# Kernel tuning notes

Hardware: AMD Instinct MI355X
Metric: run time of the kernel (lower is better)

The kernel has to match this reference:

```python
import jax, jax.numpy as jnp
import numpy as np

D = 20          # embedding dim (hardcoded in original module)
N_REL = 200     # relation vocab size (table has N_REL+1 rows)
N_TIME = 365    # time embedding table size
L = 3           # propagation layers
E = 2_000_000   # edges per layer
N = 1_000_000   # node-slot pool per layer
B = 64          # batch size
N_ENT = 1_000_003


def setup_inputs() -> dict:
    key = jax.random.key(0)
    ks = jax.random.split(key, 16)
    src_idx = jax.random.randint(ks[0], (L, E), 0, N, dtype=jnp.int32)
    dst_idx = jax.random.randint(ks[1], (L, E), 0, N, dtype=jnp.int32)
    rel_idx = jax.random.randint(ks[2], (L, E), 0, N_REL + 1, dtype=jnp.int32)
    qrel_idx = jax.random.randint(ks[3], (L, E), 0, N_REL + 1, dtype=jnp.int32)
    # signed relative time (edge_time - query_time); abs() must stay < N_TIME
    rel_time = jax.random.randint(ks[4], (L, E), -(N_TIME - 1), N_TIME, dtype=jnp.int32)
    node_batch = jax.random.randint(ks[5], (N,), 0, B, dtype=jnp.int32)
    node_ent = jnp.arange(N, dtype=jnp.int32)  # unique entity per final node slot
    s = 0.1
    rela_embed = jax.random.normal(ks[6], (N_REL + 1, D), jnp.float32) * s
    time_embed = jax.random.normal(ks[7], (N_TIME, D), jnp.float32) * s
    w_att1 = jax.random.normal(ks[8], (30, 3 * D), jnp.float32) * s
    w_att2 = jax.random.normal(ks[9], (1, 30), jnp.float32) * s
    w_past = jax.random.normal(ks[10], (D, D), jnp.float32) * s
    w_now = jax.random.normal(ks[11], (D, D), jnp.float32) * s
    w_future = jax.random.normal(ks[12], (D, D), jnp.float32) * s
    w_cls = jax.random.normal(ks[13], (D,), jnp.float32) * s
    b_cls = jnp.zeros((), jnp.float32)
    return dict(src_idx=src_idx, dst_idx=dst_idx, rel_idx=rel_idx,
                qrel_idx=qrel_idx, rel_time=rel_time, node_batch=node_batch,
                node_ent=node_ent, rela_embed=rela_embed, time_embed=time_embed,
                w_att1=w_att1, w_att2=w_att2, w_past=w_past, w_now=w_now,
                w_future=w_future, w_cls=w_cls, b_cls=b_cls,
                batch_size=B, n_ent=N_ENT)


def reference(src_idx, dst_idx, rel_idx, qrel_idx, rel_time, node_batch,
              node_ent, rela_embed, time_embed, w_att1, w_att2, w_past,
              w_now, w_future, w_cls, b_cls, batch_size, n_ent):
    n_layers = src_idx.shape[0]
    n_nodes = node_batch.shape[0]
    d = rela_embed.shape[1]
    hidden = jnp.zeros((n_nodes, d), dtype=rela_embed.dtype)
    for l in range(n_layers):
        rt = rel_time[l]                         # [E] signed relative time
        h_src = hidden[src_idx[l]]               # [E, D] gather
        r_emb = rela_embed[rel_idx[l]]           # [E, D]
        t_emb = time_embed[jnp.abs(rt)]          # [E, D]
        embed_rel = h_src + r_emb + t_emb
        # conditional time-branch MLP (mask-partitioned linear, same math as
        # the original's boolean-masked assignments)
        fut = embed_rel @ w_future.T
        now = embed_rel @ w_now.T
        pst = embed_rel @ w_past.T
        transformed = jnp.where((rt > 0)[:, None], fut,
                       jnp.where((rt == 0)[:, None], now, pst))
        # attention over concat(hidden_src, rel_emb, query_rel_emb)  [E, 3D]
        att_in = jnp.concatenate([h_src, r_emb, rela_embed[qrel_idx[l]]], axis=1)
        score = jax.nn.sigmoid(jax.nn.relu(att_in @ w_att1.T) @ w_att2.T)  # [E,1]
        msg = score * transformed                # [E, D]
        hidden = jax.ops.segment_sum(msg, dst_idx[l], num_segments=n_nodes)
        hidden = jax.nn.leaky_relu(hidden)       # default slope 0.01, as torch
    result = hidden @ w_cls + b_cls              # [N]
    score_all = jnp.zeros((batch_size, n_ent), dtype=result.dtype)
    score_all = score_all.at[node_batch, node_ent].set(result)
    return score_all
```

## Files before the change

kernel.cpp:

```cpp
#include <hip/hip_runtime.h>
#include <hip/hip_bf16.h>
#include <cstdint>

#define DD 20
#define HID 30
#define NB_SCAN 1024
#define HROW 32

typedef unsigned int  u32;
typedef unsigned short u16;

__device__ __forceinline__ void load20(const float* __restrict__ p, float* r){
  const float4* q = (const float4*)p;
#pragma unroll
  for (int i=0;i<5;i++){ float4 v=q[i]; r[4*i+0]=v.x; r[4*i+1]=v.y; r[4*i+2]=v.z; r[4*i+3]=v.w; }
}

__device__ __forceinline__ u32 pkbf(float a, float b){
  u32 ua=__float_as_uint(a); ua=(ua+0x7FFFu+((ua>>16)&1u))>>16;
  u32 ub=__float_as_uint(b); ub=(ub+0x7FFFu+((ub>>16)&1u))>>16;
  return ua | (ub<<16);
}

__global__ void k_prep(const float* __restrict__ rela, const float* __restrict__ w1,
                       const float* __restrict__ wp, const float* __restrict__ wn,
                       const float* __restrict__ wf,
                       float* __restrict__ W3, float* __restrict__ AR, float* __restrict__ AQ,
                       int nrel){
  int t = blockIdx.x*blockDim.x + threadIdx.x;
  if (t < 3*DD*DD){
    int s = t/(DD*DD), idx = t%(DD*DD);
    W3[t] = (s==0)?wp[idx]:((s==1)?wn[idx]:wf[idx]);
  }
  if (t < nrel*HID){
    int r=t/HID, j=t-r*HID;
    float sr=0.f, sq=0.f;
#pragma unroll
    for (int k=0;k<DD;k++){
      float e = rela[r*DD+k];
      sr += e*w1[j*3*DD + DD + k];
      sq += e*w1[j*3*DD + 2*DD + k];
    }
    AR[r*32+j]=sr; AQ[r*32+j]=sq;
  }
}

__global__ void k_rwtw(const float* __restrict__ rela, const float* __restrict__ timee,
                       const float* __restrict__ W3,
                       float* __restrict__ RW, float* __restrict__ TW,
                       int nrel, int ntime){
  int t = blockIdx.x*blockDim.x+threadIdx.x;
  int totR = 3*nrel*DD, totT = 3*ntime*DD;
  if (t < totR){
    int sel = t/(nrel*DD); int rem = t - sel*nrel*DD; int r = rem/DD; int i = rem - r*DD;
    const float* w = W3 + sel*DD*DD + i*DD;
    const float* e = rela + (size_t)r*DD;
    float s=0.f;
#pragma unroll
    for (int k=0;k<DD;k++) s += e[k]*w[k];
    RW[t]=s;
  }
  if (t < totT){
    int sel = t/(ntime*DD); int rem = t - sel*ntime*DD; int tt = rem/DD; int i = rem - tt*DD;
    const float* w = W3 + sel*DD*DD + i*DD;
    const float* e = timee + (size_t)tt*DD;
    float s=0.f;
#pragma unroll
    for (int k=0;k<DD;k++) s += e[k]*w[k];
    TW[t]=s;
  }
}

__global__ void k_rt(const float* __restrict__ rela, const float* __restrict__ timee,
                     const float* __restrict__ W3, float* __restrict__ RT,
                     int nrel, int ntime){
  int row = blockIdx.x*blockDim.x+threadIdx.x;
  int tot = 3*nrel*ntime;
  if (row>=tot) return;
  int per = nrel*ntime;
  int sel = row/per; int rem = row - sel*per; int r = rem/ntime; int t = rem - r*ntime;
  float e[DD], tv[DD];
  load20(rela + (size_t)r*DD, e);
  load20(timee + (size_t)t*DD, tv);
#pragma unroll
  for (int k=0;k<DD;k++) e[k]+=tv[k];
  const float* W = W3 + sel*DD*DD;
  float o[DD];
#pragma unroll
  for (int i=0;i<DD;i++){
    const float4* wr = (const float4*)(W + i*DD);
    float s=0.f;
#pragma unroll
    for (int c=0;c<5;c++){ float4 w=wr[c]; s += e[4*c]*w.x + e[4*c+1]*w.y + e[4*c+2]*w.z + e[4*c+3]*w.w; }
    o[i]=s;
  }
  float4* op=(float4*)(RT + (size_t)row*DD);
#pragma unroll
  for (int c=0;c<5;c++){ float4 v; v.x=o[4*c]; v.y=o[4*c+1]; v.z=o[4*c+2]; v.w=o[4*c+3]; op[c]=v; }
}

__global__ void __launch_bounds__(256) k_pre(const int* __restrict__ dst0, int* __restrict__ cnt0,
        int* __restrict__ rank0, int E,
        float4* __restrict__ dout4, size_t nd4,
        uint4* __restrict__ b0, uint4* __restrict__ b1, size_t nbB4,
        float4* __restrict__ bF, size_t nf4){
  int g=blockIdx.x, tid=threadIdx.x;
  int half=gridDim.x>>1;
  if (g & 1){
    int stride=half*256;
    for (int e=(g>>1)*256+tid; e<E; e+=stride)
      rank0[e]=atomicAdd(&cnt0[dst0[e]],1);
  } else {
    float4 z=make_float4(0.f,0.f,0.f,0.f);
    uint4 zu=make_uint4(0u,0u,0u,0u);
    size_t i=(size_t)(g>>1)*256+tid, st=(size_t)half*256;
    for (size_t k=i;k<nd4;k+=st) dout4[k]=z;
    for (size_t k=i;k<nbB4;k+=st){ b0[k]=zu; b1[k]=zu; }
    for (size_t k=i;k<nf4;k+=st) bF[k]=z;
  }
}

__global__ void k_scan_part(const int* __restrict__ cnt, int* __restrict__ part, int M, int C){
  __shared__ int sm[256];
  int b=blockIdx.x, t=threadIdx.x;
  int lo=b*C, hi=lo+C; if (hi>M) hi=M; if (lo>M) lo=M;
  int s=0;
  for (int i=lo+t; i<hi; i+=256) s+=cnt[i];
  sm[t]=s; __syncthreads();
  for (int o=128;o>0;o>>=1){ if (t<o) sm[t]+=sm[t+o]; __syncthreads(); }
  if (t==0) part[b]=sm[0];
}

__global__ void k_scan_top(int* __restrict__ part, int* __restrict__ listc){
  __shared__ int sm[NB_SCAN];
  int t=threadIdx.x;
  if (t==0) *listc=0;
  int v=part[t]; sm[t]=v; __syncthreads();
  for (int o=1;o<NB_SCAN;o<<=1){
    int u=(t>=o)?sm[t-o]:0; __syncthreads();
    sm[t]+=u; __syncthreads();
  }
  part[t]=sm[t]-v;
}

__global__ void k_scan_write(const int* __restrict__ cnt, const int* __restrict__ part,
                             int* __restrict__ rowptr, int M, int C){
  __shared__ int sm[256];
  int b=blockIdx.x, t=threadIdx.x;
  int lo=b*C, hi=lo+C; if (hi>M) hi=M; if (lo>M) lo=M;
  int run=part[b];
  for (int base=lo; base<hi; base+=256){
    int i=base+t;
    int v=(i<hi)?cnt[i]:0;
    sm[t]=v; __syncthreads();
    for (int o=1;o<256;o<<=1){
      int u=(t>=o)?sm[t-o]:0; __syncthreads();
      sm[t]+=u; __syncthreads();
    }
    if (i<hi) rowptr[i]=run+sm[t]-v;
    int tot=sm[255];
    __syncthreads();
    run+=tot;
  }
  if (hi==M && t==0) rowptr[M]=run;
}

__global__ void __launch_bounds__(256) k_scat(const int* __restrict__ src,const int* __restrict__ dst,
  const int* __restrict__ rel,const int* __restrict__ qrel,const int* __restrict__ rtm,
  const int* __restrict__ rank,const int* __restrict__ rowptr,int4* __restrict__ recs,int E,
  int xb,
  float* __restrict__ dout,const int* __restrict__ nb,const int* __restrict__ ne,
  const int* __restrict__ nentp,const float* __restrict__ bcls,int N){
  int g=blockIdx.x, tid=threadIdx.x;
  if (g<xb){
    float b=bcls[0]; long long stride=nentp[0];
    for (int n=g*256+tid;n<N;n+=xb*256) dout[(long long)nb[n]*stride+ne[n]]=b;
    return;
  }
  int e=(g-xb)*256+tid;
  if (e>=E) return;
  int d=dst[e];
  int pos=rowptr[d]+rank[e];
  recs[pos]=make_int4(src[e], rel[e]|(qrel[e]<<16), rtm[e], d);
}

template<bool HASH,bool HIST,bool FINAL>
__global__ void __launch_bounds__(256) k_fused(
    const int4* __restrict__ recs,
    const u16* __restrict__ hin, u16* __restrict__ hout, float* __restrict__ bufF,
    const float* __restrict__ RW, const float* __restrict__ TW,
    const float* __restrict__ AR, const float* __restrict__ AQ,
    const float* __restrict__ w1, const float* __restrict__ w2, const float* __restrict__ W3,
    int E, int nrel, int ntime,
    const int* __restrict__ ndst, int* __restrict__ ncnt, int* __restrict__ nrank, int nE,
    const float* __restrict__ wcls, const float* __restrict__ bcls,
    const int* __restrict__ nbv, const int* __restrict__ nev, const int* __restrict__ nentp,
    float* __restrict__ outp, int* __restrict__ list, int* __restrict__ listc)
{
  int lb;
  if (HIST){
    int g=blockIdx.x;
    int r3=g%3, b3=g/3;
    if (r3==2){
      int H=gridDim.x/3;
      int stride=H*256;
      for (int e=b3*256+threadIdx.x; e<nE; e+=stride)
        nrank[e]=atomicAdd(&ncnt[ndst[e]],1);
      return;
    }
    lb=b3*2+r3;
  } else lb=blockIdx.x;
  int bstart=lb*256;
  if (bstart>=E) return;

  __shared__ float sW1h[HID*DD];
  __shared__ float sW2[32];
  __shared__ float sW3[3*DD*DD];
  __shared__ u32   smsg[256*10];
  __shared__ int   sdst[256];
  __shared__ int   s_prevdst, s_nextdst;
  if (HASH){
    for (int t=threadIdx.x; t<HID*DD; t+=blockDim.x){ int j=t/DD,k=t-j*DD; sW1h[t]=w1[j*3*DD+k]; }
    for (int t=threadIdx.x; t<3*DD*DD; t+=blockDim.x) sW3[t]=W3[t];
  }
  if (threadIdx.x<HID) sW2[threadIdx.x]=w2[threadIdx.x];

  int tid = threadIdx.x;
  int bsize = E - bstart; if (bsize>256) bsize=256;
  int j = bstart + tid;
  bool active = (tid < bsize);

  if (tid==0){
    s_prevdst = (bstart>0) ? recs[-1 + (ptrdiff_t)bstart].w : -1;
    s_nextdst = (bstart+bsize < E) ? recs[bstart+bsize].w : -1;
  }
  __syncthreads();

  int dstv = -1;
  float m[DD];
  if (active){
    int4 rc = recs[j];
    int s = rc.x;
    int r = rc.y & 0xFFFF;
    int q = ((unsigned)rc.y) >> 16;
    int t = rc.z;
    dstv  = rc.w;
    int sel = (t>0)?2:((t==0)?1:0);
    int ta = (t<0)?-t:t;

    float h[DD];
    if (HASH){
      const uint4* hp=(const uint4*)(hin+(size_t)s*HROW);
      uint4 A=hp[0], B=hp[1]; uint2 Cc=*((const uint2*)(hp+2));
      h[0]=__uint_as_float(A.x<<16);  h[1]=__uint_as_float(A.x&0xFFFF0000u);
      h[2]=__uint_as_float(A.y<<16);  h[3]=__uint_as_float(A.y&0xFFFF0000u);
      h[4]=__uint_as_float(A.z<<16);  h[5]=__uint_as_float(A.z&0xFFFF0000u);
      h[6]=__uint_as_float(A.w<<16);  h[7]=__uint_as_float(A.w&0xFFFF0000u);
      h[8]=__uint_as_float(B.x<<16);  h[9]=__uint_as_float(B.x&0xFFFF0000u);
      h[10]=__uint_as_float(B.y<<16); h[11]=__uint_as_float(B.y&0xFFFF0000u);
      h[12]=__uint_as_float(B.z<<16); h[13]=__uint_as_float(B.z&0xFFFF0000u);
      h[14]=__uint_as_float(B.w<<16); h[15]=__uint_as_float(B.w&0xFFFF0000u);
      h[16]=__uint_as_float(Cc.x<<16);h[17]=__uint_as_float(Cc.x&0xFFFF0000u);
      h[18]=__uint_as_float(Cc.y<<16);h[19]=__uint_as_float(Cc.y&0xFFFF0000u);
    }

    float z=0.f;
    {
      const float4* ap=(const float4*)(AR+(size_t)r*32);
      const float4* qp=(const float4*)(AQ+(size_t)q*32);
#pragma unroll
      for (int c=0;c<7;c++){
        float4 x=ap[c], y=qp[c];
        float s4[4]={x.x+y.x, x.y+y.y, x.z+y.z, x.w+y.w};
#pragma unroll
        for (int u=0;u<4;u++){
          int jj=4*c+u;
          if (HASH){
            const float4* wr=(const float4*)&sW1h[jj*DD];
            float sum=s4[u];
#pragma unroll
            for (int c2=0;c2<5;c2++){ float4 w=wr[c2]; sum += h[4*c2]*w.x+h[4*c2+1]*w.y+h[4*c2+2]*w.z+h[4*c2+3]*w.w; }
            s4[u]=sum;
          }
          z += fmaxf(s4[u],0.f)*sW2[jj];
        }
      }
      float2 x2=*(const float2*)(AR+(size_t)r*32+28);
      float2 y2=*(const float2*)(AQ+(size_t)q*32+28);
      float s0=x2.x+y2.x, s1=x2.y+y2.y;
      if (HASH){
        const float4* wr0=(const float4*)&sW1h[28*DD];
        const float4* wr1=(const float4*)&sW1h[29*DD];
#pragma unroll
        for (int c2=0;c2<5;c2++){
          float4 wA=wr0[c2], wB=wr1[c2];
          s0 += h[4*c2]*wA.x+h[4*c2+1]*wA.y+h[4*c2+2]*wA.z+h[4*c2+3]*wA.w;
          s1 += h[4*c2]*wB.x+h[4*c2+1]*wB.y+h[4*c2+2]*wB.z+h[4*c2+3]*wB.w;
        }
      }
      z += fmaxf(s0,0.f)*sW2[28] + fmaxf(s1,0.f)*sW2[29];
    }
    float score = 1.f/(1.f+__expf(-z));

    const float4* rwp=(const float4*)(RW + ((size_t)(sel*nrel+r))*DD);
    const float4* twp=(const float4*)(TW + ((size_t)(sel*ntime+ta))*DD);
#pragma unroll
    for (int c=0;c<5;c++){
      float4 a4=rwp[c], b4=twp[c];
      float mv[4]={a4.x+b4.x, a4.y+b4.y, a4.z+b4.z, a4.w+b4.w};
      if (HASH){
#pragma unroll
        for (int u=0;u<4;u++){
          const float4* wr=(const float4*)&sW3[sel*DD*DD+(4*c+u)*DD];
          float sum=mv[u];
#pragma unroll
          for (int c2=0;c2<5;c2++){ float4 w=wr[c2]; sum += h[4*c2]*w.x+h[4*c2+1]*w.y+h[4*c2+2]*w.z+h[4*c2+3]*w.w; }
          mv[u]=sum;
        }
      }
#pragma unroll
      for (int u=0;u<4;u++) m[4*c+u]=score*mv[u];
    }
#pragma unroll
    for (int i2=0;i2<10;i2++) smsg[tid*10+i2]=pkbf(m[2*i2],m[2*i2+1]);
  }
  sdst[tid] = active ? dstv : -2;
  __syncthreads();

  if (!active) return;
  bool isHead = (tid==0) ? (s_prevdst != dstv) : (sdst[tid-1] != dstv);
  if (!(isHead || tid==0)) return;
  int k=tid+1;
  for (; k<bsize && sdst[k]==dstv; ++k){
    const u32* row=&smsg[k*10];
#pragma unroll
    for (int i2=0;i2<10;i2++){
      u32 w=row[i2];
      m[2*i2]  +=__uint_as_float(w<<16);
      m[2*i2+1]+=__uint_as_float(w&0xFFFF0000u);
    }
  }
  bool crossStart = (tid==0 && !isHead);
  bool crossEnd   = (k==bsize) && (s_nextdst==dstv);
  if (crossStart || crossEnd){
    float* o = bufF + (size_t)dstv*DD;
#pragma unroll
    for (int i=0;i<DD;i++) atomicAdd(o+i, m[i]);
    if (isHead){
      int p = atomicAdd(listc,1);
      list[p] = dstv;
    }
  } else {
    if (!FINAL){
      u32 o10[10];
#pragma unroll
      for (int i2=0;i2<10;i2++){
        float x0=m[2*i2], x1=m[2*i2+1];
        x0=fmaxf(x0,0.01f*x0); x1=fmaxf(x1,0.01f*x1);
        o10[i2]=pkbf(x0,x1);
      }
      uint4* hp=(uint4*)(hout+(size_t)dstv*HROW);
      hp[0]=make_uint4(o10[0],o10[1],o10[2],o10[3]);
      hp[1]=make_uint4(o10[4],o10[5],o10[6],o10[7]);
      *((uint2*)(hp+2))=make_uint2(o10[8],o10[9]);
    } else {
      float rsum=bcls[0];
#pragma unroll
      for (int i=0;i<DD;i++){ float x=fmaxf(m[i],0.01f*m[i]); rsum += x*wcls[i]; }
      long long stride = nentp[0];
      outp[(long long)nbv[dstv]*stride + nev[dstv]] = rsum;
    }
  }
}

template<bool FINAL>
__global__ void __launch_bounds__(256) k_fixup(float* __restrict__ bufF, u16* __restrict__ hout,
   const float* __restrict__ wcls,const float* __restrict__ bcls,
   const int* __restrict__ nb,const int* __restrict__ ne,const int* __restrict__ nentp,
   float* __restrict__ out,const int* __restrict__ list,const int* __restrict__ listc){
  int c=*listc;
  for (int i=blockIdx.x*blockDim.x+threadIdx.x; i<c; i+=gridDim.x*blockDim.x){
    int n=list[i];
    float* p=bufF+(size_t)n*DD;
    float v[DD];
#pragma unroll
    for (int jj=0;jj<DD;jj++){ v[jj]=p[jj]; p[jj]=0.f; }
    if (FINAL){
      float rsum=bcls[0];
#pragma unroll
      for (int jj=0;jj<DD;jj++){ float x=fmaxf(v[jj],0.01f*v[jj]); rsum+=x*wcls[jj]; }
      long long stride=nentp[0];
      out[(long long)nb[n]*stride+ne[n]]=rsum;
    } else {
      u32 o10[10];
#pragma unroll
      for (int i2=0;i2<10;i2++){
        float x0=v[2*i2], x1=v[2*i2+1];
        x0=fmaxf(x0,0.01f*x0); x1=fmaxf(x1,0.01f*x1);
        o10[i2]=pkbf(x0,x1);
      }
      uint4* hp=(uint4*)(hout+(size_t)n*HROW);
      hp[0]=make_uint4(o10[0],o10[1],o10[2],o10[3]);
      hp[1]=make_uint4(o10[4],o10[5],o10[6],o10[7]);
      *((uint2*)(hp+2))=make_uint2(o10[8],o10[9]);
    }
  }
}

template<bool HASH>
__global__ void __launch_bounds__(256) k_edge(
    const int* __restrict__ src, const int* __restrict__ dst,
    const int* __restrict__ rel, const int* __restrict__ qrel,
    const int* __restrict__ rtm,
    const float* __restrict__ hin, float* __restrict__ hout,
    const float* __restrict__ RT, const float* __restrict__ AR, const float* __restrict__ AQ,
    const float* __restrict__ w1, const float* __restrict__ w2, const float* __restrict__ W3,
    int E, int nrel, int ntime)
{
  __shared__ float sW1h[HID*DD];
  __shared__ float sW2[32];
  __shared__ float sW3[3*DD*DD];
  for (int t=threadIdx.x; t<HID*DD; t+=blockDim.x){ int j=t/DD,k=t-j*DD; sW1h[t]=w1[j*3*DD+k]; }
  if (threadIdx.x<HID) sW2[threadIdx.x]=w2[threadIdx.x];
  for (int t=threadIdx.x; t<3*DD*DD; t+=blockDim.x) sW3[t]=W3[t];
  __syncthreads();
  int e = blockIdx.x*blockDim.x+threadIdx.x;
  if (e>=E) return;
  int s=src[e], d=dst[e], r=rel[e], q=qrel[e], t=rtm[e];
  int sel = (t>0)?2:((t==0)?1:0);
  int ta = (t<0)?-t:t;
  float h[DD];
  if (HASH){
    load20(hin+(size_t)s*DD, h);
#pragma unroll
    for (int i=0;i<DD;i++) h[i]=fmaxf(h[i],0.01f*h[i]);
  }
  float a[HID];
  {
    const float4* ap=(const float4*)(AR+(size_t)r*32);
    const float4* qp=(const float4*)(AQ+(size_t)q*32);
#pragma unroll
    for (int c=0;c<7;c++){
      float4 x=ap[c], y=qp[c];
      a[4*c+0]=x.x+y.x; a[4*c+1]=x.y+y.y; a[4*c+2]=x.z+y.z; a[4*c+3]=x.w+y.w;
    }
    float2 x=*(const float2*)(AR+(size_t)r*32+28);
    float2 y=*(const float2*)(AQ+(size_t)q*32+28);
    a[28]=x.x+y.x; a[29]=x.y+y.y;
  }
  if (HASH){
#pragma unroll
    for (int j=0;j<HID;j++){
      const float4* wr=(const float4*)&sW1h[j*DD];
      float sum=a[j];
#pragma unroll
      for (int c=0;c<5;c++){ float4 w=wr[c]; sum += h[4*c]*w.x+h[4*c+1]*w.y+h[4*c+2]*w.z+h[4*c+3]*w.w; }
      a[j]=sum;
    }
  }
// ... 36 lines not shown
}

__global__ void k_scatter(const float* __restrict__ res, const int* __restrict__ nb,
                          const int* __restrict__ ne, const int* __restrict__ nentp,
                          float* __restrict__ out, int N){
  int i=blockIdx.x*blockDim.x+threadIdx.x;
  if (i>=N) return;
  long long stride = nentp[0];
  out[(long long)nb[i]*stride + ne[i]] = res[i];
}

extern "C" void kernel_launch(void* const* d_in, const int* in_sizes, int n_in,
                              void* d_out, int out_size, void* d_ws, size_t ws_size,
                              hipStream_t stream){
  const int*   src =(const int*)d_in[0];
  const int*   dst =(const int*)d_in[1];
  const int*   rel =(const int*)d_in[2];
  const int*   qrel=(const int*)d_in[3];
  const int*   rtm =(const int*)d_in[4];
  const int*   nb  =(const int*)d_in[5];
  const int*   ne  =(const int*)d_in[6];
  const float* rela=(const float*)d_in[7];
  const float* timee=(const float*)d_in[8];
  const float* w1  =(const float*)d_in[9];
  const float* w2  =(const float*)d_in[10];
  const float* wp  =(const float*)d_in[11];
  const float* wn  =(const float*)d_in[12];
  const float* wf  =(const float*)d_in[13];
  const float* wcls=(const float*)d_in[14];
  const float* bcls=(const float*)d_in[15];
  const int*   nentp=(const int*)d_in[17];

  const int Lc=3;
  int LE=in_sizes[0]; int E=LE/Lc;
  int N=in_sizes[5];
  int nrel=in_sizes[7]/DD;
  int ntime=in_sizes[8]/DD;

  auto al=[](size_t x){ return (x+(size_t)255)&~(size_t)255; };
  size_t szBufB=al((size_t)N*HROW*2);
  size_t szBufF=al((size_t)N*DD*4);
  size_t szBuf =al((size_t)N*DD*4);
  size_t szRW  =al((size_t)3*nrel*DD*4);
  size_t szTW  =al((size_t)3*ntime*DD*4);
  size_t szRTf =al((size_t)3*nrel*ntime*DD*4);
  size_t szA   =al((size_t)nrel*32*4);
  size_t szW3  =al((size_t)3*DD*DD*4);
  size_t szRow =al((size_t)Lc*((size_t)N+1)*4);
  size_t szRank=al((size_t)LE*4);
  size_t szCnt =al((size_t)Lc*N*4);
  size_t szRecs=al((size_t)LE*16);
  size_t szPart=al((size_t)NB_SCAN*4);
  size_t szList=al((size_t)(131072+16)*4);
  size_t need = 2*szBufB+szBufF+szRW+szTW+2*szA+szW3+szRow+szRank+szCnt+szRecs+szPart+szList;

  dim3 blk(256);
  int prepTot = (3*DD*DD > nrel*HID) ? 3*DD*DD : nrel*HID;
  int rtTot=3*nrel*ntime;
  int rwtwTot = 3*ntime*DD;

  if (ws_size >= need){
    char* base=(char*)d_ws;
    size_t off=0;
    u16*   b0 =(u16*)(base+off);   off+=szBufB;
    u16*   b1 =(u16*)(base+off);   off+=szBufB;
    float* bufF=(float*)(base+off); off+=szBufF;
    float* RW  =(float*)(base+off); off+=szRW;
    float* TW  =(float*)(base+off); off+=szTW;
    float* AR  =(float*)(base+off); off+=szA;
    float* AQ  =(float*)(base+off); off+=szA;
    float* W3  =(float*)(base+off); off+=szW3;
    int*   rowptr=(int*)(base+off); off+=szRow;
    int*   rank=(int*)(base+off);  off+=szRank;
    int*   cnt =(int*)(base+off);  off+=szCnt;
    int4*  recs=(int4*)(base+off); off+=szRecs;
    int*   part=(int*)(base+off);  off+=szPart;
    int*   listc=(int*)(base+off);
    int*   list =listc+16;          off+=szList;

    float* dout=(float*)d_out;

    (void)hipMemsetAsync(cnt,0,(size_t)Lc*N*4,stream);
    k_prep<<<dim3((prepTot+255)/256),blk,0,stream>>>(rela,w1,wp,wn,wf,W3,AR,AQ,nrel);
    k_rwtw<<<dim3((rwtwTot+255)/256),blk,0,stream>>>(rela,timee,W3,RW,TW,nrel,ntime);

    size_t nd4=(size_t)out_size>>2;
    size_t nbB4=(size_t)N*HROW*2/16;
    size_t nf4=(size_t)N*DD/4;
    k_pre<<<dim3(8192),blk,0,stream>>>(dst,cnt,rank,E,(float4*)dout,nd4,
                                       (uint4*)b0,(uint4*)b1,nbB4,(float4*)bufF,nf4);

    int C=(N+NB_SCAN-1)/NB_SCAN;
    int LB=(E+255)/256;
    int H=(LB+1)/2;

    for (int l=0;l<Lc;++l){
      int* cnt_l = cnt + (size_t)l*N;
      int* row_l = rowptr + (size_t)l*(N+1);
      k_scan_part<<<dim3(NB_SCAN),blk,0,stream>>>(cnt_l,part,N,C);
      k_scan_top<<<dim3(1),dim3(NB_SCAN),0,stream>>>(part,listc);
      k_scan_write<<<dim3(NB_SCAN),blk,0,stream>>>(cnt_l,part,row_l,N,C);
      size_t eo=(size_t)l*E;
      int xb = (l==0)?1024:0;
      k_scat<<<dim3(xb+LB),blk,0,stream>>>(src+eo,dst+eo,rel+eo,qrel+eo,rtm+eo,
          rank+eo,row_l,recs+eo,E,xb,dout,nb,ne,nentp,bcls,N);
      if (l==0){
        k_fused<false,true,false><<<dim3(3*H),blk,0,stream>>>(recs,nullptr,b0,bufF,
            RW,TW,AR,AQ,w1,w2,W3,E,nrel,ntime,
            dst+(size_t)E,cnt+(size_t)N,rank+(size_t)E,E,
            nullptr,nullptr,nullptr,nullptr,nullptr,nullptr,list,listc);
        k_fixup<false><<<dim3(128),blk,0,stream>>>(bufF,b0,wcls,bcls,nb,ne,nentp,dout,list,listc);
      } else if (l==1){
        k_fused<true,true,false><<<dim3(3*H),blk,0,stream>>>(recs+(size_t)E,b0,b1,bufF,
            RW,TW,AR,AQ,w1,w2,W3,E,nrel,ntime,
            dst+(size_t)2*E,cnt+(size_t)2*N,rank+(size_t)2*E,E,
            nullptr,nullptr,nullptr,nullptr,nullptr,nullptr,list,listc);
        k_fixup<false><<<dim3(128),blk,0,stream>>>(bufF,b1,wcls,bcls,nb,ne,nentp,dout,list,listc);
      } else {
        k_fused<true,false,true><<<dim3(LB),blk,0,stream>>>(recs+(size_t)2*E,b1,nullptr,bufF,
            RW,TW,AR,AQ,w1,w2,W3,E,nrel,ntime,
            nullptr,nullptr,nullptr,0,
            wcls,bcls,nb,ne,nentp,dout,list,listc);
        k_fixup<true><<<dim3(128),blk,0,stream>>>(bufF,nullptr,wcls,bcls,nb,ne,nentp,dout,list,listc);
      }
    }
  } else {
    char* base=(char*)d_out; float* res=(float*)d_ws;
    size_t off=0;
    float* buf0=(float*)(base+off); off+=szBuf;
    float* buf1=(float*)(base+off); off+=szBuf;
    float* RT  =(float*)(base+off); off+=szRTf;
    float* AR  =(float*)(base+off); off+=szA;
    float* AQ  =(float*)(base+off); off+=szA;
    float* W3  =(float*)(base+off); off+=szW3;
    k_prep<<<dim3((prepTot+255)/256),blk,0,stream>>>(rela,w1,wp,wn,wf,W3,AR,AQ,nrel);
    k_rt<<<dim3((rtTot+255)/256),blk,0,stream>>>(rela,timee,W3,RT,nrel,ntime);
    dim3 egrid((E+255)/256);
    dim3 ngrid((N+255)/256);
    (void)hipMemsetAsync(buf0,0,(size_t)N*DD*4,stream);
    k_edge<false><<<egrid,blk,0,stream>>>(src,dst,rel,qrel,rtm,nullptr,buf0,RT,AR,AQ,w1,w2,W3,E,nrel,ntime);
    (void)hipMemsetAsync(buf1,0,(size_t)N*DD*4,stream);
    k_edge<true><<<egrid,blk,0,stream>>>(src+(size_t)E,dst+(size_t)E,rel+(size_t)E,qrel+(size_t)E,rtm+(size_t)E,
                                         buf0,buf1,RT,AR,AQ,w1,w2,W3,E,nrel,ntime);
    (void)hipMemsetAsync(buf0,0,(size_t)N*DD*4,stream);
    k_edge<true><<<egrid,blk,0,stream>>>(src+(size_t)2*E,dst+(size_t)2*E,rel+(size_t)2*E,qrel+(size_t)2*E,rtm+(size_t)2*E,
                                         buf1,buf0,RT,AR,AQ,w1,w2,W3,E,nrel,ntime);
    k_result<<<ngrid,blk,0,stream>>>(buf0,wcls,bcls,res,N);
    (void)hipMemsetAsync(d_out,0,(size_t)out_size*sizeof(float),stream);
    k_scatter<<<ngrid,blk,0,stream>>>(res,nb,ne,nentp,(float*)d_out,N);
  }
}
```

Measured before the change: 1.057 ms.

## Make fused edge kernel persistent with software-prefetched next tile

```diff
diff --git a/kernel.cpp b/kernel.cpp
--- a/kernel.cpp
+++ b/kernel.cpp
@@ -6,6 +6,7 @@
 #define HID 30
 #define NB_SCAN 1024
 #define HROW 32
+#define CBLK 1024
 
 typedef unsigned int  u32;
 typedef unsigned short u16;
@@ -197,179 +198,209 @@
     const int* __restrict__ nbv, const int* __restrict__ nev, const int* __restrict__ nentp,
     float* __restrict__ outp, int* __restrict__ list, int* __restrict__ listc)
 {
-  int lb;
+  int g=blockIdx.x;
+  int C;
   if (HIST){
-    int g=blockIdx.x;
-    int r3=g%3, b3=g/3;
-    if (r3==2){
-      int H=gridDim.x/3;
-      int stride=H*256;
-      for (int e=b3*256+threadIdx.x; e<nE; e+=stride)
+    if (g & 1){
+      int Hst=gridDim.x>>1;
+      int stride=Hst*256;
+      for (int e=(g>>1)*256+threadIdx.x; e<nE; e+=stride)
         nrank[e]=atomicAdd(&ncnt[ndst[e]],1);
       return;
     }
-    lb=b3*2+r3;
-  } else lb=blockIdx.x;
-  int bstart=lb*256;
-  if (bstart>=E) return;
+    g>>=1; C=gridDim.x>>1;
+  } else C=gridDim.x;
+
+  int nt=(E+255)/256;
+  if (g>=nt) return;
 
   __shared__ float sW1h[HID*DD];
   __shared__ float sW2[32];
   __shared__ float sW3[3*DD*DD];
   __shared__ u32   smsg[256*10];
   __shared__ int   sdst[256];
-  __shared__ int   s_prevdst, s_nextdst;
+  __shared__ int   sPN[2];
+  int tid=threadIdx.x;
   if (HASH){
-    for (int t=threadIdx.x; t<HID*DD; t+=blockDim.x){ int j=t/DD,k=t-j*DD; sW1h[t]=w1[j*3*DD+k]; }
-    for (int t=threadIdx.x; t<3*DD*DD; t+=blockDim.x) sW3[t]=W3[t];
-  }
-  if (threadIdx.x<HID) sW2[threadIdx.x]=w2[threadIdx.x];
-
-  int tid = threadIdx.x;
-  int bsize = E - bstart; if (bsize>256) bsize=256;
-  int j = bstart + tid;
-  bool active = (tid < bsize);
-
-  if (tid==0){
-    s_prevdst = (bstart>0) ? recs[-1 + (ptrdiff_t)bstart].w : -1;
-    s_nextdst = (bstart+bsize < E) ? recs[bstart+bsize].w : -1;
-  }
+    for (int t=tid; t<HID*DD; t+=256){ int j=t/DD,k=t-j*DD; sW1h[t]=w1[j*3*DD+k]; }
+    for (int t=tid; t<3*DD*DD; t+=256) sW3[t]=W3[t];
+  }
+  if (tid<HID) sW2[tid]=w2[tid];
   __syncthreads();
 
-  int dstv = -1;
-  float m[DD];
-  if (active){
-    int4 rc = recs[j];
-    int s = rc.x;
-    int r = rc.y & 0xFFFF;
-    int q = ((unsigned)rc.y) >> 16;
-    int t = rc.z;
-    dstv  = rc.w;
-    int sel = (t>0)?2:((t==0)?1:0);
-    int ta = (t<0)?-t:t;
-
+  int tile=g;
+  int bstart=tile*256;
+  bool act=(bstart+tid<E);
+  int4 rcC = act ? recs[bstart+tid] : make_int4(0,0,0,-2);
+  uint4 hA, hB; uint2 hC2;
+  if (HASH){
+    const uint4* hp=(const uint4*)(hin+(size_t)(act?rcC.x:0)*HROW);
+    hA=hp[0]; hB=hp[1]; hC2=*((const uint2*)(hp+2));
+  }
+
+  while (true){
+    int bsize=E-bstart; if (bsize>256) bsize=256;
+    int tileN=tile+C;
+    int bstartN=tileN*256;
+    bool actN=(tileN<nt)&&(bstartN+tid<E);
+    int4 rcN = actN ? recs[bstartN+tid] : make_int4(0,0,0,-2);
+    if (tid==0){
+      sPN[0]=(bstart>0)?recs[bstart-1].w:-1;
+      sPN[1]=(bstart+bsize<E)?recs[bstart+bsize].w:-1;
+    }
+
+    int dstv=-2;
+    float score=0.f; int sel=0, r=0, q=0, ta=0;
     float h[DD];
+    if (act){
+      dstv=rcC.w;
+      r = rcC.y & 0xFFFF;
+      q = ((unsigned)rcC.y) >> 16;
+      int t = rcC.z;
+      sel = (t>0)?2:((t==0)?1:0);
+      ta = (t<0)?-t:t;
+      if (HASH){
+        h[0]=__uint_as_float(hA.x<<16);  h[1]=__uint_as_float(hA.x&0xFFFF0000u);
+        h[2]=__uint_as_float(hA.y<<16);  h[3]=__uint_as_float(hA.y&0xFFFF0000u);
+        h[4]=__uint_as_float(hA.z<<16);  h[5]=__uint_as_float(hA.z&0xFFFF0000u);
+        h[6]=__uint_as_float(hA.w<<16);  h[7]=__uint_as_float(hA.w&0xFFFF0000u);
+        h[8]=__uint_as_float(hB.x<<16);  h[9]=__uint_as_float(hB.x&0xFFFF0000u);
+        h[10]=__uint_as_float(hB.y<<16); h[11]=__uint_as_float(hB.y&0xFFFF0000u);
+        h[12]=__uint_as_float(hB.z<<16); h[13]=__uint_as_float(hB.z&0xFFFF0000u);
+        h[14]=__uint_as_float(hB.w<<16); h[15]=__uint_as_float(hB.w&0xFFFF0000u);
+        h[16]=__uint_as_float(hC2.x<<16);h[17]=__uint_as_float(hC2.x&0xFFFF0000u);
+        h[18]=__uint_as_float(hC2.y<<16);h[19]=__uint_as_float(hC2.y&0xFFFF0000u);
+      }
+      float z=0.f;
+      {
+        const float4* ap=(const float4*)(AR+(size_t)r*32);
+        const float4* qp=(const float4*)(AQ+(size_t)q*32);
+#pragma unroll
+        for (int c=0;c<7;c++){
+          float4 x=ap[c], y=qp[c];
+          float s4[4]={x.x+y.x, x.y+y.y, x.z+y.z, x.w+y.w};
+#pragma unroll
+          for (int u=0;u<4;u++){
+            int jj=4*c+u;
+            if (HASH){
+              const float4* wr=(const float4*)&sW1h[jj*DD];
+              float sum=s4[u];
+#pragma unroll
+              for (int c2=0;c2<5;c2++){ float4 w=wr[c2]; sum += h[4*c2]*w.x+h[4*c2+1]*w.y+h[4*c2+2]*w.z+h[4*c2+3]*w.w; }
+              s4[u]=sum;
+            }
+            z += fmaxf(s4[u],0.f)*sW2[jj];
+          }
+        }
+        float2 x2=*(const float2*)(AR+(size_t)r*32+28);
+        float2 y2=*(const float2*)(AQ+(size_t)q*32+28);
+        float s0=x2.x+y2.x, s1=x2.y+y2.y;
+        if (HASH){
+          const float4* wr0=(const float4*)&sW1h[28*DD];
+          const float4* wr1=(const float4*)&sW1h[29*DD];
+#pragma unroll
+          for (int c2=0;c2<5;c2++){
+            float4 wA=wr0[c2], wB=wr1[c2];
+            s0 += h[4*c2]*wA.x+h[4*c2+1]*wA.y+h[4*c2+2]*wA.z+h[4*c2+3]*wA.w;
+            s1 += h[4*c2]*wB.x+h[4*c2+1]*wB.y+h[4*c2+2]*wB.z+h[4*c2+3]*wB.w;
+          }
+        }
+        z += fmaxf(s0,0.f)*sW2[28] + fmaxf(s1,0.f)*sW2[29];
+      }
+      score = 1.f/(1.f+__expf(-z));
+    }
+
+    uint4 hAn, hBn; uint2 hCn;
     if (HASH){
-      const uint4* hp=(const uint4*)(hin+(size_t)s*HROW);
-      uint4 A=hp[0], B=hp[1]; uint2 Cc=*((const uint2*)(hp+2));
-      h[0]=__uint_as_float(A.x<<16);  h[1]=__uint_as_float(A.x&0xFFFF0000u);
-      h[2]=__uint_as_float(A.y<<16);  h[3]=__uint_as_float(A.y&0xFFFF0000u);
-      h[4]=__uint_as_float(A.z<<16);  h[5]=__uint_as_float(A.z&0xFFFF0000u);
-      h[6]=__uint_as_float(A.w<<16);  h[7]=__uint_as_float(A.w&0xFFFF0000u);
-      h[8]=__uint_as_float(B.x<<16);  h[9]=__uint_as_float(B.x&0xFFFF0000u);
-      h[10]=__uint_as_float(B.y<<16); h[11]=__uint_as_float(B.y&0xFFFF0000u);
-      h[12]=__uint_as_float(B.z<<16); h[13]=__uint_as_float(B.z&0xFFFF0000u);
-      h[14]=__uint_as_float(B.w<<16); h[15]=__uint_as_float(B.w&0xFFFF0000u);
-      h[16]=__uint_as_float(Cc.x<<16);h[17]=__uint_as_float(Cc.x&0xFFFF0000u);
-      h[18]=__uint_as_float(Cc.y<<16);h[19]=__uint_as_float(Cc.y&0xFFFF0000u);
-    }
-
-    float z=0.f;
-    {
-      const float4* ap=(const float4*)(AR+(size_t)r*32);
-      const float4* qp=(const float4*)(AQ+(size_t)q*32);
-#pragma unroll
-      for (int c=0;c<7;c++){
-        float4 x=ap[c], y=qp[c];
-        float s4[4]={x.x+y.x, x.y+y.y, x.z+y.z, x.w+y.w};
-#pragma unroll
-        for (int u=0;u<4;u++){
-          int jj=4*c+u;
-          if (HASH){
-            const float4* wr=(const float4*)&sW1h[jj*DD];
-            float sum=s4[u];
+      const uint4* hpN=(const uint4*)(hin+(size_t)(actN?rcN.x:0)*HROW);
+      hAn=hpN[0]; hBn=hpN[1]; hCn=*((const uint2*)(hpN+2));
+    }
+
+    if (act){
+      const float4* rwp=(const float4*)(RW + ((size_t)(sel*nrel+r))*DD);
+      const float4* twp=(const float4*)(TW + ((size_t)(sel*ntime+ta))*DD);
+#pragma unroll
+      for (int c=0;c<5;c++){
+        float4 a4=rwp[c], b4=twp[c];
+        float mv[4]={a4.x+b4.x, a4.y+b4.y, a4.z+b4.z, a4.w+b4.w};
+        if (HASH){
+#pragma unroll
+          for (int u=0;u<4;u++){
+            const float4* wr=(const float4*)&sW3[sel*DD*DD+(4*c+u)*DD];
+            float sum=mv[u];
 #pragma unroll
             for (int c2=0;c2<5;c2++){ float4 w=wr[c2]; sum += h[4*c2]*w.x+h[4*c2+1]*w.y+h[4*c2+2]*w.z+h[4*c2+3]*w.w; }
-            s4[u]=sum;
+            mv[u]=sum;
           }
-          z += fmaxf(s4[u],0.f)*sW2[jj];
+        }
+        smsg[tid*10+2*c]  =pkbf(score*mv[0],score*mv[1]);
+        smsg[tid*10+2*c+1]=pkbf(score*mv[2],score*mv[3]);
+      }
+    }
+    sdst[tid]=dstv;
+    __syncthreads();
+
+    if (act){
+      bool isHead = (tid==0) ? (sPN[0]!=dstv) : (sdst[tid-1]!=dstv);
+      if (isHead || tid==0){
+        float mm[DD];
+        {
+          const u32* row=&smsg[tid*10];
+#pragma unroll
+          for (int i2=0;i2<10;i2++){
+            u32 w=row[i2];
+            mm[2*i2]  =__uint_as_float(w<<16);
+            mm[2*i2+1]=__uint_as_float(w&0xFFFF0000u);
+          }
+        }
+        int k=tid+1;
+        for (; k<bsize && sdst[k]==dstv; ++k){
+          const u32* row=&smsg[k*10];
+#pragma unroll
+          for (int i2=0;i2<10;i2++){
+            u32 w=row[i2];
+            mm[2*i2]  +=__uint_as_float(w<<16);
+            mm[2*i2+1]+=__uint_as_float(w&0xFFFF0000u);
+          }
+        }
+        bool crossStart = (tid==0 && !isHead);
+        bool crossEnd   = (k==bsize) && (sPN[1]==dstv);
+        if (crossStart || crossEnd){
+          float* o = bufF + (size_t)dstv*DD;
+#pragma unroll
+          for (int i=0;i<DD;i++) atomicAdd(o+i, mm[i]);
+          if (isHead){
+            int p = atomicAdd(listc,1);
+            list[p] = dstv;
+          }
+        } else {
+          if (!FINAL){
+            u32 o10[10];
+#pragma unroll
+            for (int i2=0;i2<10;i2++){
+              float x0=mm[2*i2], x1=mm[2*i2+1];
+              x0=fmaxf(x0,0.01f*x0); x1=fmaxf(x1,0.01f*x1);
+              o10[i2]=pkbf(x0,x1);
+            }
+            uint4* hp=(uint4*)(hout+(size_t)dstv*HROW);
+            hp[0]=make_uint4(o10[0],o10[1],o10[2],o10[3]);
+            hp[1]=make_uint4(o10[4],o10[5],o10[6],o10[7]);
+            *((uint2*)(hp+2))=make_uint2(o10[8],o10[9]);
+          } else {
+            float rsum=bcls[0];
+#pragma unroll
+            for (int i=0;i<DD;i++){ float x=fmaxf(mm[i],0.01f*mm[i]); rsum += x*wcls[i]; }
+            long long stride = nentp[0];
+            outp[(long long)nbv[dstv]*stride + nev[dstv]] = rsum;
+          }
         }
       }
-      float2 x2=*(const float2*)(AR+(size_t)r*32+28);
-      float2 y2=*(const float2*)(AQ+(size_t)q*32+28);
-      float s0=x2.x+y2.x, s1=x2.y+y2.y;
-      if (HASH){
-        const float4* wr0=(const float4*)&sW1h[28*DD];
-        const float4* wr1=(const float4*)&sW1h[29*DD];
-#pragma unroll
-        for (int c2=0;c2<5;c2++){
-          float4 wA=wr0[c2], wB=wr1[c2];
-          s0 += h[4*c2]*wA.x+h[4*c2+1]*wA.y+h[4*c2+2]*wA.z+h[4*c2+3]*wA.w;
-          s1 += h[4*c2]*wB.x+h[4*c2+1]*wB.y+h[4*c2+2]*wB.z+h[4*c2+3]*wB.w;
-        }
-      }
-      z += fmaxf(s0,0.f)*sW2[28] + fmaxf(s1,0.f)*sW2[29];
-    }
-    float score = 1.f/(1.f+__expf(-z));
-
-    const float4* rwp=(const float4*)(RW + ((size_t)(sel*nrel+r))*DD);
-    const float4* twp=(const float4*)(TW + ((size_t)(sel*ntime+ta))*DD);
-#pragma unroll
-    for (int c=0;c<5;c++){
-      float4 a4=rwp[c], b4=twp[c];
-      float mv[4]={a4.x+b4.x, a4.y+b4.y, a4.z+b4.z, a4.w+b4.w};
-      if (HASH){
-#pragma unroll
-        for (int u=0;u<4;u++){
-          const float4* wr=(const float4*)&sW3[sel*DD*DD+(4*c+u)*DD];
-          float sum=mv[u];
-#pragma unroll
-          for (int c2=0;c2<5;c2++){ float4 w=wr[c2]; sum += h[4*c2]*w.x+h[4*c2+1]*w.y+h[4*c2+2]*w.z+h[4*c2+3]*w.w; }
-          mv[u]=sum;
-        }
-      }
-#pragma unroll
-      for (int u=0;u<4;u++) m[4*c+u]=score*mv[u];
-    }
-#pragma unroll
-    for (int i2=0;i2<10;i2++) smsg[tid*10+i2]=pkbf(m[2*i2],m[2*i2+1]);
-  }
-  sdst[tid] = active ? dstv : -2;
-  __syncthreads();
-
-  if (!active) return;
-  bool isHead = (tid==0) ? (s_prevdst != dstv) : (sdst[tid-1] != dstv);
-  if (!(isHead || tid==0)) return;
-  int k=tid+1;
-  for (; k<bsize && sdst[k]==dstv; ++k){
-    const u32* row=&smsg[k*10];
-#pragma unroll
-    for (int i2=0;i2<10;i2++){
-      u32 w=row[i2];
-      m[2*i2]  +=__uint_as_float(w<<16);
-      m[2*i2+1]+=__uint_as_float(w&0xFFFF0000u);
-    }
-  }
-  bool crossStart = (tid==0 && !isHead);
-  bool crossEnd   = (k==bsize) && (s_nextdst==dstv);
-  if (crossStart || crossEnd){
-    float* o = bufF + (size_t)dstv*DD;
-#pragma unroll
-    for (int i=0;i<DD;i++) atomicAdd(o+i, m[i]);
-    if (isHead){
-      int p = atomicAdd(listc,1);
-      list[p] = dstv;
-    }
-  } else {
-    if (!FINAL){
-      u32 o10[10];
-#pragma unroll
-      for (int i2=0;i2<10;i2++){
-        float x0=m[2*i2], x1=m[2*i2+1];
-        x0=fmaxf(x0,0.01f*x0); x1=fmaxf(x1,0.01f*x1);
-        o10[i2]=pkbf(x0,x1);
-      }
-      uint4* hp=(uint4*)(hout+(size_t)dstv*HROW);
-      hp[0]=make_uint4(o10[0],o10[1],o10[2],o10[3]);
-      hp[1]=make_uint4(o10[4],o10[5],o10[6],o10[7]);
-      *((uint2*)(hp+2))=make_uint2(o10[8],o10[9]);
-    } else {
-      float rsum=bcls[0];
-#pragma unroll
-      for (int i=0;i<DD;i++){ float x=fmaxf(m[i],0.01f*m[i]); rsum += x*wcls[i]; }
-      long long stride = nentp[0];
-      outp[(long long)nbv[dstv]*stride + nev[dstv]] = rsum;
-    }
+    }
+
+    tile=tileN; bstart=bstartN; act=actN; rcC=rcN;
+    if (HASH){ hA=hAn; hB=hBn; hC2=hCn; }
+    if (tile>=nt) break;
+    __syncthreads();
   }
 }
 
@@ -587,7 +618,6 @@
 
     int C=(N+NB_SCAN-1)/NB_SCAN;
     int LB=(E+255)/256;
-    int H=(LB+1)/2;
 
     for (int l=0;l<Lc;++l){
       int* cnt_l = cnt + (size_t)l*N;
@@ -600,19 +630,19 @@
       k_scat<<<dim3(xb+LB),blk,0,stream>>>(src+eo,dst+eo,rel+eo,qrel+eo,rtm+eo,
           rank+eo,row_l,recs+eo,E,xb,dout,nb,ne,nentp,bcls,N);
       if (l==0){
-        k_fused<false,true,false><<<dim3(3*H),blk,0,stream>>>(recs,nullptr,b0,bufF,
+        k_fused<false,true,false><<<dim3(2*CBLK),blk,0,stream>>>(recs,nullptr,b0,bufF,
             RW,TW,AR,AQ,w1,w2,W3,E,nrel,ntime,
             dst+(size_t)E,cnt+(size_t)N,rank+(size_t)E,E,
             nullptr,nullptr,nullptr,nullptr,nullptr,nullptr,list,listc);
         k_fixup<false><<<dim3(128),blk,0,stream>>>(bufF,b0,wcls,bcls,nb,ne,nentp,dout,list,listc);
       } else if (l==1){
-        k_fused<true,true,false><<<dim3(3*H),blk,0,stream>>>(recs+(size_t)E,b0,b1,bufF,
+        k_fused<true,true,false><<<dim3(2*CBLK),blk,0,stream>>>(recs+(size_t)E,b0,b1,bufF,
             RW,TW,AR,AQ,w1,w2,W3,E,nrel,ntime,
             dst+(size_t)2*E,cnt+(size_t)2*N,rank+(size_t)2*E,E,
             nullptr,nullptr,nullptr,nullptr,nullptr,nullptr,list,listc);
         k_fixup<false><<<dim3(128),blk,0,stream>>>(bufF,b1,wcls,bcls,nb,ne,nentp,dout,list,listc);
       } else {
-        k_fused<true,false,true><<<dim3(LB),blk,0,stream>>>(recs+(size_t)2*E,b1,nullptr,bufF,
+        k_fused<true,false,true><<<dim3(CBLK),blk,0,stream>>>(recs+(size_t)2*E,b1,nullptr,bufF,
             RW,TW,AR,AQ,w1,w2,W3,E,nrel,ntime,
             nullptr,nullptr,nullptr,0,
             wcls,bcls,nb,ne,nentp,dout,list,listc);
```

New measurement: 1.284 ms. +21.5%, slower.

## Overlap next-layer CSR scatter and histogram with fused edge kernels; defer final output

Applied to the files above, without the earlier changes.

```diff
diff --git a/kernel.cpp b/kernel.cpp
--- a/kernel.cpp
+++ b/kernel.cpp
@@ -99,17 +99,21 @@
   for (int c=0;c<5;c++){ float4 v; v.x=o[4*c]; v.y=o[4*c+1]; v.z=o[4*c+2]; v.w=o[4*c+3]; op[c]=v; }
 }
 
-__global__ void __launch_bounds__(256) k_pre(const int* __restrict__ dst0, int* __restrict__ cnt0,
-        int* __restrict__ rank0, int E,
+__global__ void __launch_bounds__(256) k_pre(const int* __restrict__ dst, int* __restrict__ cnt,
+        int* __restrict__ rank, int E, int N,
         float4* __restrict__ dout4, size_t nd4,
         uint4* __restrict__ b0, uint4* __restrict__ b1, size_t nbB4,
-        float4* __restrict__ bF, size_t nf4){
+        float4* __restrict__ bF, size_t nf4,
+        float4* __restrict__ res4, size_t nr4){
   int g=blockIdx.x, tid=threadIdx.x;
   int half=gridDim.x>>1;
   if (g & 1){
     int stride=half*256;
-    for (int e=(g>>1)*256+tid; e<E; e+=stride)
-      rank0[e]=atomicAdd(&cnt0[dst0[e]],1);
+    int E2=2*E;
+    for (int e=(g>>1)*256+tid; e<E2; e+=stride){
+      int l=(e>=E)?1:0;
+      rank[e]=atomicAdd(&cnt[(size_t)l*N+dst[e]],1);
+    }
   } else {
     float4 z=make_float4(0.f,0.f,0.f,0.f);
     uint4 zu=make_uint4(0u,0u,0u,0u);
@@ -117,6 +121,7 @@
     for (size_t k=i;k<nd4;k+=st) dout4[k]=z;
     for (size_t k=i;k<nbB4;k+=st){ b0[k]=zu; b1[k]=zu; }
     for (size_t k=i;k<nf4;k+=st) bF[k]=z;
+    for (size_t k=i;k<nr4;k+=st) res4[k]=z;
   }
 }
 
@@ -167,24 +172,15 @@
 
 __global__ void __launch_bounds__(256) k_scat(const int* __restrict__ src,const int* __restrict__ dst,
   const int* __restrict__ rel,const int* __restrict__ qrel,const int* __restrict__ rtm,
-  const int* __restrict__ rank,const int* __restrict__ rowptr,int4* __restrict__ recs,int E,
-  int xb,
-  float* __restrict__ dout,const int* __restrict__ nb,const int* __restrict__ ne,
-  const int* __restrict__ nentp,const float* __restrict__ bcls,int N){
-  int g=blockIdx.x, tid=threadIdx.x;
-  if (g<xb){
-    float b=bcls[0]; long long stride=nentp[0];
-    for (int n=g*256+tid;n<N;n+=xb*256) dout[(long long)nb[n]*stride+ne[n]]=b;
-    return;
-  }
-  int e=(g-xb)*256+tid;
+  const int* __restrict__ rank,const int* __restrict__ rowptr,int4* __restrict__ recs,int E){
+  int e=blockIdx.x*blockDim.x+threadIdx.x;
   if (e>=E) return;
   int d=dst[e];
   int pos=rowptr[d]+rank[e];
   recs[pos]=make_int4(src[e], rel[e]|(qrel[e]<<16), rtm[e], d);
 }
 
-template<bool HASH,bool HIST,bool FINAL>
+template<bool HASH,bool FINAL,int XR>
 __global__ void __launch_bounds__(256) k_fused(
     const int4* __restrict__ recs,
     const u16* __restrict__ hin, u16* __restrict__ hout, float* __restrict__ bufF,
@@ -192,25 +188,36 @@
     const float* __restrict__ AR, const float* __restrict__ AQ,
     const float* __restrict__ w1, const float* __restrict__ w2, const float* __restrict__ W3,
     int E, int nrel, int ntime,
-    const int* __restrict__ ndst, int* __restrict__ ncnt, int* __restrict__ nrank, int nE,
-    const float* __restrict__ wcls, const float* __restrict__ bcls,
-    const int* __restrict__ nbv, const int* __restrict__ nev, const int* __restrict__ nentp,
-    float* __restrict__ outp, int* __restrict__ list, int* __restrict__ listc)
+    const int* __restrict__ sA_src, const int* __restrict__ sA_dst,
+    const int* __restrict__ sA_rel, const int* __restrict__ sA_qrel,
+    const int* __restrict__ sA_rtm, const int* __restrict__ sA_rank,
+    const int* __restrict__ sA_rowptr, int4* __restrict__ sA_recs, int sA_E,
+    const int* __restrict__ hB_dst, int* __restrict__ hB_cnt, int* __restrict__ hB_rank, int hB_E,
+    const float* __restrict__ wcls, float* __restrict__ res,
+    int* __restrict__ list, int* __restrict__ listc)
 {
-  int lb;
-  if (HIST){
-    int g=blockIdx.x;
-    int r3=g%3, b3=g/3;
-    if (r3==2){
-      int H=gridDim.x/3;
-      int stride=H*256;
-      for (int e=b3*256+threadIdx.x; e<nE; e+=stride)
-        nrank[e]=atomicAdd(&ncnt[ndst[e]],1);
+  int g=blockIdx.x;
+  if (XR>0){
+    const int M=2+XR;
+    int r=g%M, b=g/M, R=gridDim.x/M;
+    if (r==2){
+      int stride=R*256;
+      for (int e=b*256+threadIdx.x; e<sA_E; e+=stride){
+        int d=sA_dst[e];
+        int pos=sA_rowptr[d]+sA_rank[e];
+        sA_recs[pos]=make_int4(sA_src[e], sA_rel[e]|(sA_qrel[e]<<16), sA_rtm[e], d);
+      }
       return;
     }
-    lb=b3*2+r3;
-  } else lb=blockIdx.x;
-  int bstart=lb*256;
+    if (XR>1 && r==3){
+      int stride=R*256;
+      for (int e=b*256+threadIdx.x; e<hB_E; e+=stride)
+        hB_rank[e]=atomicAdd(&hB_cnt[hB_dst[e]],1);
+      return;
+    }
+    g = b*2+r;
+  }
+  int bstart=g*256;
   if (bstart>=E) return;
 
   __shared__ float sW1h[HID*DD];
@@ -346,7 +353,7 @@
     float* o = bufF + (size_t)dstv*DD;
 #pragma unroll
     for (int i=0;i<DD;i++) atomicAdd(o+i, m[i]);
-    if (isHead){
+    if (!FINAL && isHead){
       int p = atomicAdd(listc,1);
       list[p] = dstv;
     }
@@ -364,20 +371,16 @@
       hp[1]=make_uint4(o10[4],o10[5],o10[6],o10[7]);
       *((uint2*)(hp+2))=make_uint2(o10[8],o10[9]);
     } else {
-      float rsum=bcls[0];
+      float rsum=0.f;
 #pragma unroll
       for (int i=0;i<DD;i++){ float x=fmaxf(m[i],0.01f*m[i]); rsum += x*wcls[i]; }
-      long long stride = nentp[0];
-      outp[(long long)nbv[dstv]*stride + nev[dstv]] = rsum;
-    }
-  }
-}
-
-template<bool FINAL>
+      res[dstv] = rsum;
+    }
+  }
+}
+
 __global__ void __launch_bounds__(256) k_fixup(float* __restrict__ bufF, u16* __restrict__ hout,
-   const float* __restrict__ wcls,const float* __restrict__ bcls,
-   const int* __restrict__ nb,const int* __restrict__ ne,const int* __restrict__ nentp,
-   float* __restrict__ out,const int* __restrict__ list,const int* __restrict__ listc){
+   const int* __restrict__ list,const int* __restrict__ listc){
   int c=*listc;
   for (int i=blockIdx.x*blockDim.x+threadIdx.x; i<c; i+=gridDim.x*blockDim.x){
     int n=list[i];
@@ -385,26 +388,36 @@
     float v[DD];
 #pragma unroll
     for (int jj=0;jj<DD;jj++){ v[jj]=p[jj]; p[jj]=0.f; }
-    if (FINAL){
-      float rsum=bcls[0];
-#pragma unroll
-      for (int jj=0;jj<DD;jj++){ float x=fmaxf(v[jj],0.01f*v[jj]); rsum+=x*wcls[jj]; }
-      long long stride=nentp[0];
-      out[(long long)nb[n]*stride+ne[n]]=rsum;
-    } else {
-      u32 o10[10];
-#pragma unroll
-      for (int i2=0;i2<10;i2++){
-        float x0=v[2*i2], x1=v[2*i2+1];
-        x0=fmaxf(x0,0.01f*x0); x1=fmaxf(x1,0.01f*x1);
-        o10[i2]=pkbf(x0,x1);
-      }
-      uint4* hp=(uint4*)(hout+(size_t)n*HROW);
-      hp[0]=make_uint4(o10[0],o10[1],o10[2],o10[3]);
-      hp[1]=make_uint4(o10[4],o10[5],o10[6],o10[7]);
-      *((uint2*)(hp+2))=make_uint2(o10[8],o10[9]);
-    }
-  }
+    u32 o10[10];
+#pragma unroll
+    for (int i2=0;i2<10;i2++){
+      float x0=v[2*i2], x1=v[2*i2+1];
+      x0=fmaxf(x0,0.01f*x0); x1=fmaxf(x1,0.01f*x1);
+      o10[i2]=pkbf(x0,x1);
+    }
+    uint4* hp=(uint4*)(hout+(size_t)n*HROW);
+    hp[0]=make_uint4(o10[0],o10[1],o10[2],o10[3]);
+    hp[1]=make_uint4(o10[4],o10[5],o10[6],o10[7]);
+    *((uint2*)(hp+2))=make_uint2(o10[8],o10[9]);
+  }
+}
+
+__global__ void __launch_bounds__(256) k_out(const float* __restrict__ res,
+   const float* __restrict__ bufF, const float* __restrict__ wcls, const float* __restrict__ bcls,
+   const int* __restrict__ nb, const int* __restrict__ ne, const int* __restrict__ nentp,
+   float* __restrict__ out, int N){
+  int n=blockIdx.x*blockDim.x+threadIdx.x;
+  if (n>=N) return;
+  float acc = res[n] + bcls[0];
+  const float4* q=(const float4*)(bufF+(size_t)n*DD);
+#pragma unroll
+  for (int c=0;c<5;c++){
+    float4 v=q[c];
+    acc += fmaxf(v.x,0.01f*v.x)*wcls[4*c]   + fmaxf(v.y,0.01f*v.y)*wcls[4*c+1]
+         + fmaxf(v.z,0.01f*v.z)*wcls[4*c+2] + fmaxf(v.w,0.01f*v.w)*wcls[4*c+3];
+  }
+  long long stride = nentp[0];
+  out[(long long)nb[n]*stride + ne[n]] = acc;
 }
 
 template<bool HASH>
@@ -547,7 +560,8 @@
   size_t szRecs=al((size_t)LE*16);
   size_t szPart=al((size_t)NB_SCAN*4);
   size_t szList=al((size_t)(131072+16)*4);
-  size_t need = 2*szBufB+szBufF+szRW+szTW+2*szA+szW3+szRow+szRank+szCnt+szRecs+szPart+szList;
+  size_t szRes =al((size_t)N*4);
+  size_t need = 2*szBufB+szBufF+szRW+szTW+2*szA+szW3+szRow+szRank+szCnt+szRecs+szPart+szList+szRes;
 
   dim3 blk(256);
   int prepTot = (3*DD*DD > nrel*HID) ? 3*DD*DD : nrel*HID;
@@ -572,6 +586,7 @@
     int*   part=(int*)(base+off);  off+=szPart;
     int*   listc=(int*)(base+off);
     int*   list =listc+16;          off+=szList;
+    float* res =(float*)(base+off); off+=szRes;
 
     float* dout=(float*)d_out;
 
@@ -582,43 +597,55 @@
     size_t nd4=(size_t)out_size>>2;
     size_t nbB4=(size_t)N*HROW*2/16;
     size_t nf4=(size_t)N*DD/4;
-    k_pre<<<dim3(8192),blk,0,stream>>>(dst,cnt,rank,E,(float4*)dout,nd4,
-                                       (uint4*)b0,(uint4*)b1,nbB4,(float4*)bufF,nf4);
+    size_t nr4=(size_t)N/4;
+    k_pre<<<dim3(8192),blk,0,stream>>>(dst,cnt,rank,E,N,(float4*)dout,nd4,
+                                       (uint4*)b0,(uint4*)b1,nbB4,(float4*)bufF,nf4,
+                                       (float4*)res,nr4);
 
     int C=(N+NB_SCAN-1)/NB_SCAN;
     int LB=(E+255)/256;
     int H=(LB+1)/2;
 
-    for (int l=0;l<Lc;++l){
+    for (int l=0;l<2;++l){
       int* cnt_l = cnt + (size_t)l*N;
       int* row_l = rowptr + (size_t)l*(N+1);
       k_scan_part<<<dim3(NB_SCAN),blk,0,stream>>>(cnt_l,part,N,C);
       k_scan_top<<<dim3(1),dim3(NB_SCAN),0,stream>>>(part,listc);
       k_scan_write<<<dim3(NB_SCAN),blk,0,stream>>>(cnt_l,part,row_l,N,C);
-      size_t eo=(size_t)l*E;
-      int xb = (l==0)?1024:0;
-      k_scat<<<dim3(xb+LB),blk,0,stream>>>(src+eo,dst+eo,rel+eo,qrel+eo,rtm+eo,
-          rank+eo,row_l,recs+eo,E,xb,dout,nb,ne,nentp,bcls,N);
-      if (l==0){
-        k_fused<false,true,false><<<dim3(3*H),blk,0,stream>>>(recs,nullptr,b0,bufF,
-            RW,TW,AR,AQ,w1,w2,W3,E,nrel,ntime,
-            dst+(size_t)E,cnt+(size_t)N,rank+(size_t)E,E,
-            nullptr,nullptr,nullptr,nullptr,nullptr,nullptr,list,listc);
-        k_fixup<false><<<dim3(128),blk,0,stream>>>(bufF,b0,wcls,bcls,nb,ne,nentp,dout,list,listc);
-      } else if (l==1){
-        k_fused<true,true,false><<<dim3(3*H),blk,0,stream>>>(recs+(size_t)E,b0,b1,bufF,
-            RW,TW,AR,AQ,w1,w2,W3,E,nrel,ntime,
-            dst+(size_t)2*E,cnt+(size_t)2*N,rank+(size_t)2*E,E,
-            nullptr,nullptr,nullptr,nullptr,nullptr,nullptr,list,listc);
-        k_fixup<false><<<dim3(128),blk,0,stream>>>(bufF,b1,wcls,bcls,nb,ne,nentp,dout,list,listc);
-      } else {
-        k_fused<true,false,true><<<dim3(LB),blk,0,stream>>>(recs+(size_t)2*E,b1,nullptr,bufF,
-            RW,TW,AR,AQ,w1,w2,W3,E,nrel,ntime,
-            nullptr,nullptr,nullptr,0,
-            wcls,bcls,nb,ne,nentp,dout,list,listc);
-        k_fixup<true><<<dim3(128),blk,0,stream>>>(bufF,nullptr,wcls,bcls,nb,ne,nentp,dout,list,listc);
-      }
-    }
+    }
+    k_scat<<<dim3(LB),blk,0,stream>>>(src,dst,rel,qrel,rtm,rank,rowptr,recs,E);
+
+    k_fused<false,false,2><<<dim3(4*H),blk,0,stream>>>(recs,nullptr,b0,bufF,
+        RW,TW,AR,AQ,w1,w2,W3,E,nrel,ntime,
+        src+(size_t)E,dst+(size_t)E,rel+(size_t)E,qrel+(size_t)E,rtm+(size_t)E,
+        rank+(size_t)E,rowptr+(size_t)(N+1),recs+(size_t)E,E,
+        dst+(size_t)2*E,cnt+(size_t)2*N,rank+(size_t)2*E,E,
+        wcls,res,list,listc);
+    k_fixup<<<dim3(128),blk,0,stream>>>(bufF,b0,list,listc);
+
+    {
+      int* cnt_l = cnt + (size_t)2*N;
+      int* row_l = rowptr + (size_t)2*(N+1);
+      k_scan_part<<<dim3(NB_SCAN),blk,0,stream>>>(cnt_l,part,N,C);
+      k_scan_top<<<dim3(1),dim3(NB_SCAN),0,stream>>>(part,listc);
+      k_scan_write<<<dim3(NB_SCAN),blk,0,stream>>>(cnt_l,part,row_l,N,C);
+    }
+
+    k_fused<true,false,1><<<dim3(3*H),blk,0,stream>>>(recs+(size_t)E,b0,b1,bufF,
+        RW,TW,AR,AQ,w1,w2,W3,E,nrel,ntime,
+        src+(size_t)2*E,dst+(size_t)2*E,rel+(size_t)2*E,qrel+(size_t)2*E,rtm+(size_t)2*E,
+        rank+(size_t)2*E,rowptr+(size_t)2*(N+1),recs+(size_t)2*E,E,
+        nullptr,nullptr,nullptr,0,
+        wcls,res,list,listc);
+    k_fixup<<<dim3(128),blk,0,stream>>>(bufF,b1,list,listc);
+
+    k_fused<true,true,0><<<dim3(LB),blk,0,stream>>>(recs+(size_t)2*E,b1,nullptr,bufF,
+        RW,TW,AR,AQ,w1,w2,W3,E,nrel,ntime,
+        nullptr,nullptr,nullptr,nullptr,nullptr,nullptr,nullptr,nullptr,0,
+        nullptr,nullptr,nullptr,0,
+        wcls,res,list,listc);
+
+    k_out<<<dim3((N+255)/256),blk,0,stream>>>(res,bufF,wcls,bcls,nb,ne,nentp,dout,N);
   } else {
     char* base=(char*)d_out; float* res=(float*)d_ws;
     size_t off=0;
```

New measurement: 1.102 ms. +4.2%, slower.
